# Kernel tuning notes

Measured on AMD Instinct MI355X. Metric: run time of the kernel, lower is better.

## Reference

```python
import jax, jax.numpy as jnp
import numpy as np


def setup_inputs() -> dict:
    key = jax.random.key(0)
    k1, k2, k3 = jax.random.split(key, 3)
    B, S, D, L = 8, 512, 512, 32
    head = jax.random.normal(k1, (B, S, D), dtype=jnp.float32)
    dep = jax.random.normal(k2, (B, S, D), dtype=jnp.float32)
    label_U_diag = jax.random.normal(k3, (L, D), dtype=jnp.float32)
    return {"head": head, "dep": dep, "label_U_diag": label_U_diag}


def reference(head, dep, label_U_diag):
    # head: [b, i, j], label_U_diag: [l, j], dep: [b, o, j] -> [b, l, i, o]
    return jnp.einsum('bij,lj,boj->blio', head, label_U_diag, dep)
```

## Files before the change

kernel.cpp:

```cpp
#include <hip/hip_runtime.h>
#include <hip/hip_bf16.h>

typedef float f32x4  __attribute__((ext_vector_type(4)));
typedef short bf16x8 __attribute__((ext_vector_type(8)));

__device__ __forceinline__ short bf16r(float x) {
    unsigned u = __builtin_bit_cast(unsigned, x);
    u += 0x7fffu + ((u >> 16) & 1u);
    return (short)(u >> 16);
}

__global__ void cvt_kernel(const float* __restrict__ head, const float* __restrict__ dep,
                           short* __restrict__ hb, short* __restrict__ db) {
    const int n8 = 8 * 512 * 512 / 8;
    int i = blockIdx.x * blockDim.x + threadIdx.x;
    const float* src = (i < n8) ? head : dep;
    short* dst = (i < n8) ? hb : db;
    int j = (i < n8) ? i : i - n8;
    f32x4 a = *(const f32x4*)(src + (size_t)j * 8);
    f32x4 c = *(const f32x4*)(src + (size_t)j * 8 + 4);
    bf16x8 v;
#pragma unroll
    for (int e = 0; e < 4; ++e) { v[e] = bf16r(a[e]); v[4 + e] = bf16r(c[e]); }
    *(bf16x8*)(dst + (size_t)j * 8) = v;
}

__global__ __launch_bounds__(512, 2)
void bla_gemm3(const short* __restrict__ headb,
               const short* __restrict__ depb,
               const float* __restrict__ U,
               float* __restrict__ out)
{
    constexpr int S = 512, D = 512, L = 32, BM = 256, BN = 256, BK = 64, NT = 8;

    __shared__ __align__(16) short Al[2][BM * BK];
    __shared__ __align__(16) short Bl[2][BN * BK];

    const int tid = threadIdx.x, lane = tid & 63, wid = tid >> 6;
    const int wm = wid >> 2, wn = wid & 3;

    const int swz = (blockIdx.x & 7) * ((int)gridDim.x >> 3) + (blockIdx.x >> 3);
    const int b = swz >> 7, rem = swz & 127;
    const int it = rem >> 6, l = (rem >> 1) & 31, ot = rem & 1;
    const int i0 = it * BM, o0 = ot * BN;

    const int ar = tid >> 3, ac = (tid & 7) * 8;
    const short* hbase = headb + (size_t)(b * S + i0 + ar) * D + ac;
    const float* ubase = U + (size_t)l * D + ac;
    const int awoff = ((((tid & 7) * 16) ^ ((ar & 7) << 4)) >> 1);

    const int bso = ((lane & 7) * 16) ^ ((lane >> 3) << 4);
    const short* dbase = depb + (size_t)(b * S + o0) * D;

    bf16x8 rA[4];
    float  ruf[8];

#define A_ISSUE(t_) do {                                                        \
        _Pragma("unroll")                                                       \
        for (int p = 0; p < 4; ++p)                                             \
            rA[p] = *(const bf16x8*)(hbase + (size_t)(p * 64) * D + (t_) * BK); \
        f32x4 u0 = *(const f32x4*)(ubase + (t_) * BK);                          \
        f32x4 u1 = *(const f32x4*)(ubase + (t_) * BK + 4);                      \
        _Pragma("unroll")                                                       \
        for (int e = 0; e < 4; ++e) { ruf[e] = u0[e]; ruf[4 + e] = u1[e]; }     \
    } while (0)

#define A_WRITE(buf_) do {                                                      \
        _Pragma("unroll")                                                       \
        for (int p = 0; p < 4; ++p) {                                           \
            bf16x8 av;                                                          \
            _Pragma("unroll")                                                   \
            for (int e = 0; e < 8; ++e) {                                       \
                float f = __builtin_bit_cast(float,                             \
                    (unsigned)((unsigned short)rA[p][e]) << 16) * ruf[e];       \
                av[e] = bf16r(f);                                               \
            }                                                                   \
            *(bf16x8*)&Al[buf_][(ar + p * 64) * BK + awoff] = av;               \
        }                                                                       \
    } while (0)

#define B_ISSUE(t_, buf_) do {                                                  \
        _Pragma("unroll")                                                       \
        for (int q = 0; q < 4; ++q) {                                           \
            const int rg = wid * 32 + q * 8 + (lane >> 3);                      \
            const char* s_ = (const char*)dbase +                               \
                ((size_t)rg * D + (size_t)(t_) * BK) * 2 + bso;                 \
            __builtin_amdgcn_global_load_lds(                                   \
                (const __attribute__((address_space(1))) void*)s_,              \
                (__attribute__((address_space(3))) void*)&Bl[buf_][(wid * 32 + q * 8) * BK], \
                16, 0, 0);                                                      \
        }                                                                       \
    } while (0)

    f32x4 acc[8][4] = {};
    bf16x8 bfr[4];

#define DSREAD_A(buf_, mh_, ks_, af_) do {                                      \
        const int cb = (ks_) * 64 + ((lane >> 4) << 4);                         \
        _Pragma("unroll")                                                       \
        for (int f = 0; f < 4; ++f) {                                           \
            const int row = wm * 128 + ((mh_) * 4 + f) * 16 + (lane & 15);      \
            af_[f] = *(const bf16x8*)&Al[buf_][row * BK + ((cb ^ ((row & 7) << 4)) >> 1)]; \
        }                                                                       \
    } while (0)

#define DSREAD_B(buf_, ks_) do {                                                \
        const int cb = (ks_) * 64 + ((lane >> 4) << 4);                         \
        _Pragma("unroll")                                                       \
        for (int f = 0; f < 4; ++f) {                                           \
            const int row = wn * 64 + f * 16 + (lane & 15);                     \
            bfr[f] = *(const bf16x8*)&Bl[buf_][row * BK + ((cb ^ ((row & 7) << 4)) >> 1)]; \
        }                                                                       \
    } while (0)

#define MFMA16(mh_, af_) do {                                                   \
        __builtin_amdgcn_s_setprio(1);                                          \
        _Pragma("unroll")                                                       \
        for (int m = 0; m < 4; ++m)                                             \
            _Pragma("unroll")                                                   \
            for (int n = 0; n < 4; ++n)                                         \
                acc[(mh_) * 4 + m][n] = __builtin_amdgcn_mfma_f32_16x16x32_bf16(\
                    af_[m], bfr[n], acc[(mh_) * 4 + m][n], 0, 0, 0);            \
        __builtin_amdgcn_s_setprio(0);                                          \
    } while (0)

#define SB()  __builtin_amdgcn_sched_barrier(0)
#define BAR() __builtin_amdgcn_s_barrier()

    A_ISSUE(0);
    B_ISSUE(0, 0);
    A_WRITE(0);
    asm volatile("s_waitcnt vmcnt(0) lgkmcnt(0)");
    BAR();

#pragma unroll
    for (int t = 0; t < NT; ++t) {
        const int c = t & 1;
        bf16x8 af[4];
        if (t < NT - 1) { A_ISSUE(t + 1); B_ISSUE(t + 1, c ^ 1); }
        DSREAD_A(c, 0, 0, af); DSREAD_B(c, 0);
        SB(); BAR();
        MFMA16(0, af);
        SB(); BAR();
        DSREAD_A(c, 1, 0, af);
        SB(); BAR();
        MFMA16(1, af);
        SB(); BAR();
        if (t < NT - 1) A_WRITE(c ^ 1);
        DSREAD_A(c, 0, 1, af); DSREAD_B(c, 1);
        SB(); BAR();
        MFMA16(0, af);
        SB(); BAR();
        DSREAD_A(c, 1, 1, af);
        SB(); BAR();
        MFMA16(1, af);
        SB();
        asm volatile("s_waitcnt vmcnt(0) lgkmcnt(0)");
        BAR();
    }

    float* op = out + (size_t)(b * L + l) * S * S;
#pragma unroll
    for (int m = 0; m < 8; ++m) {
        const int row0 = i0 + wm * 128 + m * 16 + ((lane >> 4) << 2);
#pragma unroll
        for (int n = 0; n < 4; ++n) {
            const int col = o0 + wn * 64 + n * 16 + (lane & 15);
#pragma unroll
            for (int r = 0; r < 4; ++r)
                op[(size_t)(row0 + r) * S + col] = acc[m][n][r];
        }
    }

#undef A_ISSUE
#undef A_WRITE
#undef B_ISSUE
#undef DSREAD_A
#undef DSREAD_B
#undef MFMA16
#undef SB
#undef BAR
}

__global__ __launch_bounds__(256, 2)
void bla_fb(const float* __restrict__ head, const float* __restrict__ dep,
            const float* __restrict__ U, float* __restrict__ out)
{
    constexpr int S = 512, D = 512, L = 32, BM = 128, BN = 128, BK = 64, NT = 8;
    __shared__ short Al[2][BM * BK];
    __shared__ short Bl[2][BN * BK];
    const int tid = threadIdx.x, lane = tid & 63, wid = tid >> 6;
    const int wm = wid >> 1, wn = wid & 1;
    const int swz = (blockIdx.x & 7) * ((int)gridDim.x >> 3) + (blockIdx.x >> 3);
    const int b = swz >> 9, rem = swz & 511;
    const int l = rem >> 4, it = (rem >> 2) & 3, ot = rem & 3;
    const int i0 = it * BM, o0 = ot * BN;
    const int srow = tid >> 3, scol = (tid & 7) * 8, swb = scol * 2;
    const float* hb = head + (size_t)(b * S + i0 + srow) * D + scol;
    const float* db = dep + (size_t)(b * S + o0 + srow) * D + scol;
    const float* ub = U + l * D + scol;
    f32x4 ra[4][2], rb[4][2], ru[2];
#define FSTAGE_LOAD(t) do { const int k0_ = (t) * BK;                              \
        ru[0] = *(const f32x4*)(ub + k0_); ru[1] = *(const f32x4*)(ub + k0_ + 4);  \
        _Pragma("unroll") for (int p_ = 0; p_ < 4; ++p_) {                         \
            ra[p_][0] = *(const f32x4*)(hb + k0_ + p_ * 32 * D);                   \
            ra[p_][1] = *(const f32x4*)(hb + k0_ + p_ * 32 * D + 4);               \
            rb[p_][0] = *(const f32x4*)(db + k0_ + p_ * 32 * D);                   \
            rb[p_][1] = *(const f32x4*)(db + k0_ + p_ * 32 * D + 4); } } while (0)
#define FSTAGE_WRITE(buf) do { _Pragma("unroll") for (int p_ = 0; p_ < 4; ++p_) {  \
            const int row_ = srow + p_ * 32; const int sb_ = swb ^ ((row_ & 7) << 4); \
            bf16x8 av_, bv_;                                                       \
            _Pragma("unroll") for (int q_ = 0; q_ < 2; ++q_)                       \
                _Pragma("unroll") for (int j_ = 0; j_ < 4; ++j_) {                 \
                    av_[q_ * 4 + j_] = bf16r(ra[p_][q_][j_] * ru[q_][j_]);         \
                    bv_[q_ * 4 + j_] = bf16r(rb[p_][q_][j_]); }                    \
            *(bf16x8*)&Al[buf][row_ * BK + (sb_ >> 1)] = av_;                      \
            *(bf16x8*)&Bl[buf][row_ * BK + (sb_ >> 1)] = bv_; } } while (0)
    f32x4 acc[4][4] = {};
    const int cbase = (lane >> 4) << 4, rsw = (lane & 7) << 4;
#define FCOMPUTE(buf) do { _Pragma("unroll") for (int ks_ = 0; ks_ < 2; ++ks_) {   \
            const int sb2_ = (ks_ * 64 + cbase) ^ rsw; bf16x8 af_[4], bfr_[4];     \
            _Pragma("unroll") for (int f_ = 0; f_ < 4; ++f_) {                     \
                af_[f_] = *(const bf16x8*)&Al[buf][(wm * 64 + f_ * 16 + (lane & 15)) * BK + (sb2_ >> 1)]; \
                bfr_[f_] = *(const bf16x8*)&Bl[buf][(wn * 64 + f_ * 16 + (lane & 15)) * BK + (sb2_ >> 1)]; } \
            _Pragma("unroll") for (int fm_ = 0; fm_ < 4; ++fm_)                    \
                _Pragma("unroll") for (int fn_ = 0; fn_ < 4; ++fn_)                \
                    acc[fm_][fn_] = __builtin_amdgcn_mfma_f32_16x16x32_bf16(       \
                        af_[fm_], bfr_[fn_], acc[fm_][fn_], 0, 0, 0); } } while (0)
    FSTAGE_LOAD(0); FSTAGE_WRITE(0); __syncthreads();
    int cur = 0;
#pragma unroll
    for (int t = 0; t < NT; ++t) {
        if (t + 1 < NT) FSTAGE_LOAD(t + 1);
        FCOMPUTE(cur);
        if (t + 1 < NT) FSTAGE_WRITE(cur ^ 1);
        __syncthreads();
        cur ^= 1;
    }
    float* op = out + (size_t)(b * L + l) * S * S;
#pragma unroll
    for (int fm = 0; fm < 4; ++fm) {
        const int row0 = i0 + wm * 64 + fm * 16 + ((lane >> 4) << 2);
#pragma unroll
        for (int fn = 0; fn < 4; ++fn) {
            const int col = o0 + wn * 64 + fn * 16 + (lane & 15);
#pragma unroll
            for (int r = 0; r < 4; ++r)
                op[(size_t)(row0 + r) * S + col] = acc[fm][fn][r];
        }
    }
#undef FSTAGE_LOAD
#undef FSTAGE_WRITE
#undef FCOMPUTE
}

extern "C" void kernel_launch(void* const* d_in, const int* in_sizes, int n_in,
                              void* d_out, int out_size, void* d_ws, size_t ws_size,
                              hipStream_t stream)
{
    const float* head = (const float*)d_in[0];
    const float* dep  = (const float*)d_in[1];
    const float* U    = (const float*)d_in[2];
    float* out        = (float*)d_out;

    const size_t nelem = (size_t)8 * 512 * 512;
    const size_t need  = nelem * 2 * 2;
    if (ws_size >= need) {
        short* headb = (short*)d_ws;
        short* depb  = headb + nelem;
        cvt_kernel<<<dim3(2048), dim3(256), 0, stream>>>(head, dep, headb, depb);
        bla_gemm3<<<dim3(1024), dim3(512), 0, stream>>>(headb, depb, U, out);
    } else {
        bla_fb<<<dim3(4096), dim3(256), 0, stream>>>(head, dep, U, out);
    }
}
```

Measured before the change: 127.3 us.

## Deepen A-operand register prefetch to two stages and interleave B loads with MFMA phases

The main GEMM now holds two register stages of head/U tiles, so global loads for tile t+2 are issued while tile t is computed. The B global-to-LDS loads and the A scale-and-write into LDS are split into halves and spread across the four MFMA phases of each iteration. The per-iteration wait becomes a partial vmcnt so the newest prefetch can stay in flight across the barrier. This aims to hide global-load latency behind the matrix cores, at the cost of higher register pressure and fragile hand-written wait counts. The bf16 rounding also switches to the __float2bfloat16 intrinsic.

```diff
diff --git a/kernel.cpp b/kernel.cpp
--- a/kernel.cpp
+++ b/kernel.cpp
@@ -26,7 +26,7 @@
 }
 
 __global__ __launch_bounds__(512, 2)
-void bla_gemm3(const short* __restrict__ headb,
+void bla_gemm4(const short* __restrict__ headb,
                const short* __restrict__ depb,
                const float* __restrict__ U,
                float* __restrict__ out)
@@ -52,42 +52,45 @@
     const int bso = ((lane & 7) * 16) ^ ((lane >> 3) << 4);
     const short* dbase = depb + (size_t)(b * S + o0) * D;
 
-    bf16x8 rA[4];
-    float  ruf[8];
-
-#define A_ISSUE(t_) do {                                                        \
+    bf16x8 rA[2][4];
+    f32x4  ru[2][2];
+
+#define SBAR() __builtin_amdgcn_sched_barrier(0)
+
+#define A_ISSUE(tt) do {                                                        \
+        const int s_ = (tt) & 1;                                                \
         _Pragma("unroll")                                                       \
         for (int p = 0; p < 4; ++p)                                             \
-            rA[p] = *(const bf16x8*)(hbase + (size_t)(p * 64) * D + (t_) * BK); \
-        f32x4 u0 = *(const f32x4*)(ubase + (t_) * BK);                          \
-        f32x4 u1 = *(const f32x4*)(ubase + (t_) * BK + 4);                      \
-        _Pragma("unroll")                                                       \
-        for (int e = 0; e < 4; ++e) { ruf[e] = u0[e]; ruf[4 + e] = u1[e]; }     \
-    } while (0)
-
-#define A_WRITE(buf_) do {                                                      \
-        _Pragma("unroll")                                                       \
-        for (int p = 0; p < 4; ++p) {                                           \
+            rA[s_][p] = *(const bf16x8*)(hbase + (size_t)(p * 64) * D + (tt) * BK); \
+        ru[s_][0] = *(const f32x4*)(ubase + (tt) * BK);                         \
+        ru[s_][1] = *(const f32x4*)(ubase + (tt) * BK + 4);                     \
+    } while (0)
+
+#define A_WRITE_H(tt, h) do {                                                   \
+        const int s_ = (tt) & 1;                                                \
+        _Pragma("unroll")                                                       \
+        for (int p = (h) * 2; p < (h) * 2 + 2; ++p) {                           \
             bf16x8 av;                                                          \
             _Pragma("unroll")                                                   \
             for (int e = 0; e < 8; ++e) {                                       \
                 float f = __builtin_bit_cast(float,                             \
-                    (unsigned)((unsigned short)rA[p][e]) << 16) * ruf[e];       \
-                av[e] = bf16r(f);                                               \
+                    (unsigned)((unsigned short)rA[s_][p][e]) << 16)             \
+                    * ru[s_][e >> 2][e & 3];                                    \
+                av[e] = __builtin_bit_cast(short, __float2bfloat16(f));         \
             }                                                                   \
-            *(bf16x8*)&Al[buf_][(ar + p * 64) * BK + awoff] = av;               \
-        }                                                                       \
-    } while (0)
-
-#define B_ISSUE(t_, buf_) do {                                                  \
-        _Pragma("unroll")                                                       \
-        for (int q = 0; q < 4; ++q) {                                           \
+            *(bf16x8*)&Al[s_][(ar + p * 64) * BK + awoff] = av;                 \
+        }                                                                       \
+    } while (0)
+
+#define B_ISSUE_H(tt, h) do {                                                   \
+        _Pragma("unroll")                                                       \
+        for (int q = (h) * 2; q < (h) * 2 + 2; ++q) {                           \
             const int rg = wid * 32 + q * 8 + (lane >> 3);                      \
             const char* s_ = (const char*)dbase +                               \
-                ((size_t)rg * D + (size_t)(t_) * BK) * 2 + bso;                 \
+                ((size_t)rg * D + (size_t)(tt) * BK) * 2 + bso;                 \
             __builtin_amdgcn_global_load_lds(                                   \
                 (const __attribute__((address_space(1))) void*)s_,              \
-                (__attribute__((address_space(3))) void*)&Bl[buf_][(wid * 32 + q * 8) * BK], \
+                (__attribute__((address_space(3))) void*)&Bl[(tt) & 1][(wid * 32 + q * 8) * BK], \
                 16, 0, 0);                                                      \
         }                                                                       \
     } while (0)
@@ -124,39 +127,54 @@
         __builtin_amdgcn_s_setprio(0);                                          \
     } while (0)
 
-#define SB()  __builtin_amdgcn_sched_barrier(0)
 #define BAR() __builtin_amdgcn_s_barrier()
 
     A_ISSUE(0);
-    B_ISSUE(0, 0);
-    A_WRITE(0);
-    asm volatile("s_waitcnt vmcnt(0) lgkmcnt(0)");
+    B_ISSUE_H(0, 0); B_ISSUE_H(0, 1);
+    SBAR();
+    A_WRITE_H(0, 0); A_WRITE_H(0, 1);
+    A_ISSUE(1);
+    SBAR();
+    asm volatile("s_waitcnt vmcnt(6) lgkmcnt(0)" ::: "memory");
+    SBAR();
     BAR();
+    SBAR();
 
 #pragma unroll
     for (int t = 0; t < NT; ++t) {
         const int c = t & 1;
         bf16x8 af[4];
-        if (t < NT - 1) { A_ISSUE(t + 1); B_ISSUE(t + 1, c ^ 1); }
+
         DSREAD_A(c, 0, 0, af); DSREAD_B(c, 0);
-        SB(); BAR();
+        if (t + 1 < NT) B_ISSUE_H(t + 1, 0);
+        SBAR(); BAR(); SBAR();
         MFMA16(0, af);
-        SB(); BAR();
+        SBAR(); BAR(); SBAR();
+
         DSREAD_A(c, 1, 0, af);
-        SB(); BAR();
+        if (t + 1 < NT) B_ISSUE_H(t + 1, 1);
+        SBAR(); BAR(); SBAR();
         MFMA16(1, af);
-        SB(); BAR();
-        if (t < NT - 1) A_WRITE(c ^ 1);
+        SBAR(); BAR(); SBAR();
+
         DSREAD_A(c, 0, 1, af); DSREAD_B(c, 1);
-        SB(); BAR();
+        if (t + 1 < NT) A_WRITE_H(t + 1, 0);
+        SBAR(); BAR(); SBAR();
         MFMA16(0, af);
-        SB(); BAR();
+        SBAR(); BAR(); SBAR();
+
         DSREAD_A(c, 1, 1, af);
-        SB(); BAR();
+        if (t + 1 < NT) A_WRITE_H(t + 1, 1);
+        if (t + 2 < NT) A_ISSUE(t + 2);
+        SBAR(); BAR(); SBAR();
         MFMA16(1, af);
-        SB();
-        asm volatile("s_waitcnt vmcnt(0) lgkmcnt(0)");
-        BAR();
+        SBAR();
+        if (t + 2 < NT) {
+            asm volatile("s_waitcnt vmcnt(6) lgkmcnt(0)" ::: "memory");
+        } else if (t + 1 < NT) {
+            asm volatile("s_waitcnt vmcnt(0) lgkmcnt(0)" ::: "memory");
+        }
+        SBAR(); BAR(); SBAR();
     }
 
     float* op = out + (size_t)(b * L + l) * S * S;
@@ -172,13 +190,13 @@
         }
     }
 
+#undef SBAR
 #undef A_ISSUE
-#undef A_WRITE
-#undef B_ISSUE
+#undef A_WRITE_H
+#undef B_ISSUE_H
 #undef DSREAD_A
 #undef DSREAD_B
 #undef MFMA16
-#undef SB
 #undef BAR
 }
 
@@ -269,7 +287,7 @@
         short* headb = (short*)d_ws;
         short* depb  = headb + nelem;
         cvt_kernel<<<dim3(2048), dim3(256), 0, stream>>>(head, dep, headb, depb);
-        bla_gemm3<<<dim3(1024), dim3(512), 0, stream>>>(headb, depb, U, out);
+        bla_gemm4<<<dim3(1024), dim3(512), 0, stream>>>(headb, depb, U, out);
     } else {
         bla_fb<<<dim3(4096), dim3(256), 0, stream>>>(head, dep, U, out);
     }
```

Measured after the change: 111.4 us. 12.5% less time.

## Load A fragments directly into registers, dropping A's LDS staging

Applied to the files above, without the earlier changes.

The A operand (head scaled by U[l]) is no longer written to shared memory. Each wave now loads its MFMA A fragments straight from global memory, scales them in registers and rounds to bf16. The wave layout changes to 4x2 with 64x128 per-wave tiles, so each wave reads more B fragments from LDS and reuses A across 8 columns. Most intra-iteration barriers are removed, leaving one per K-step. In exchange there are more scattered global loads for A, higher register pressure, and less latency hiding because every K-step waits on vmcnt(0).

```diff
diff --git a/kernel.cpp b/kernel.cpp
--- a/kernel.cpp
+++ b/kernel.cpp
@@ -26,160 +26,159 @@
 }
 
 __global__ __launch_bounds__(512, 2)
-void bla_gemm3(const short* __restrict__ headb,
+void bla_gemm6(const short* __restrict__ headb,
                const short* __restrict__ depb,
                const float* __restrict__ U,
                float* __restrict__ out)
 {
     constexpr int S = 512, D = 512, L = 32, BM = 256, BN = 256, BK = 64, NT = 8;
 
-    __shared__ __align__(16) short Al[2][BM * BK];
     __shared__ __align__(16) short Bl[2][BN * BK];
 
     const int tid = threadIdx.x, lane = tid & 63, wid = tid >> 6;
-    const int wm = wid >> 2, wn = wid & 3;
+    const int wm = wid >> 1, wn = wid & 1;
 
     const int swz = (blockIdx.x & 7) * ((int)gridDim.x >> 3) + (blockIdx.x >> 3);
     const int b = swz >> 7, rem = swz & 127;
     const int it = rem >> 6, l = (rem >> 1) & 31, ot = rem & 1;
     const int i0 = it * BM, o0 = ot * BN;
 
-    const int ar = tid >> 3, ac = (tid & 7) * 8;
-    const short* hbase = headb + (size_t)(b * S + i0 + ar) * D + ac;
-    const float* ubase = U + (size_t)l * D + ac;
-    const int awoff = ((((tid & 7) * 16) ^ ((ar & 7) << 4)) >> 1);
+    const short* hfrag = headb + (size_t)(b * S + i0 + wm * 64 + (lane & 15)) * D
+                         + ((lane >> 4) * 8);
+    const float* ubase = U + (size_t)l * D + ((lane >> 4) * 8);
 
     const int bso = ((lane & 7) * 16) ^ ((lane >> 3) << 4);
     const short* dbase = depb + (size_t)(b * S + o0) * D;
 
-    bf16x8 rA[4];
-    float  ruf[8];
-
-#define A_ISSUE(t_) do {                                                        \
-        _Pragma("unroll")                                                       \
-        for (int p = 0; p < 4; ++p)                                             \
-            rA[p] = *(const bf16x8*)(hbase + (size_t)(p * 64) * D + (t_) * BK); \
-        f32x4 u0 = *(const f32x4*)(ubase + (t_) * BK);                          \
-        f32x4 u1 = *(const f32x4*)(ubase + (t_) * BK + 4);                      \
-        _Pragma("unroll")                                                       \
-        for (int e = 0; e < 4; ++e) { ruf[e] = u0[e]; ruf[4 + e] = u1[e]; }     \
-    } while (0)
-
-#define A_WRITE(buf_) do {                                                      \
-        _Pragma("unroll")                                                       \
-        for (int p = 0; p < 4; ++p) {                                           \
-            bf16x8 av;                                                          \
-            _Pragma("unroll")                                                   \
-            for (int e = 0; e < 8; ++e) {                                       \
-                float f = __builtin_bit_cast(float,                             \
-                    (unsigned)((unsigned short)rA[p][e]) << 16) * ruf[e];       \
-                av[e] = bf16r(f);                                               \
-            }                                                                   \
-            *(bf16x8*)&Al[buf_][(ar + p * 64) * BK + awoff] = av;               \
-        }                                                                       \
-    } while (0)
-
-#define B_ISSUE(t_, buf_) do {                                                  \
+    bf16x8 rw[2][4];
+    bf16x8 sc[2][4];
+    f32x4  uf[2][2];
+    bf16x8 bfr[8];
+    f32x4  acc[4][8] = {};
+
+#define SB()  __builtin_amdgcn_sched_barrier(0)
+#define BAR() __builtin_amdgcn_s_barrier()
+
+#define B_ISSUE(tt) do {                                                        \
         _Pragma("unroll")                                                       \
         for (int q = 0; q < 4; ++q) {                                           \
             const int rg = wid * 32 + q * 8 + (lane >> 3);                      \
             const char* s_ = (const char*)dbase +                               \
-                ((size_t)rg * D + (size_t)(t_) * BK) * 2 + bso;                 \
+                ((size_t)rg * D + (size_t)(tt) * BK) * 2 + bso;                 \
             __builtin_amdgcn_global_load_lds(                                   \
                 (const __attribute__((address_space(1))) void*)s_,              \
-                (__attribute__((address_space(3))) void*)&Bl[buf_][(wid * 32 + q * 8) * BK], \
+                (__attribute__((address_space(3))) void*)&Bl[(tt) & 1][(wid * 32 + q * 8) * BK], \
                 16, 0, 0);                                                      \
         }                                                                       \
     } while (0)
 
-    f32x4 acc[8][4] = {};
-    bf16x8 bfr[4];
-
-#define DSREAD_A(buf_, mh_, ks_, af_) do {                                      \
-        const int cb = (ks_) * 64 + ((lane >> 4) << 4);                         \
-        _Pragma("unroll")                                                       \
-        for (int f = 0; f < 4; ++f) {                                           \
-            const int row = wm * 128 + ((mh_) * 4 + f) * 16 + (lane & 15);      \
-            af_[f] = *(const bf16x8*)&Al[buf_][row * BK + ((cb ^ ((row & 7) << 4)) >> 1)]; \
-        }                                                                       \
+#define AQ_ISSUE(tt, ks) do {                                                   \
+        _Pragma("unroll")                                                       \
+        for (int mf = 0; mf < 4; ++mf)                                          \
+            rw[ks][mf] = *(const bf16x8*)(hfrag + (size_t)(mf * 16) * D +       \
+                                          (tt) * BK + (ks) * 32);               \
+    } while (0)
+
+#define U_ISSUE(tt) do {                                                        \
+        _Pragma("unroll")                                                       \
+        for (int ks = 0; ks < 2; ++ks)                                          \
+            _Pragma("unroll")                                                   \
+            for (int h = 0; h < 2; ++h)                                         \
+                uf[ks][h] = *(const f32x4*)(ubase + (tt) * BK + ks * 32 + h * 4);\
+    } while (0)
+
+#define SCALE_ALL() do {                                                        \
+        _Pragma("unroll")                                                       \
+        for (int ks = 0; ks < 2; ++ks)                                          \
+            _Pragma("unroll")                                                   \
+            for (int mf = 0; mf < 4; ++mf) {                                    \
+                bf16x8 av;                                                      \
+                _Pragma("unroll")                                               \
+                for (int e = 0; e < 8; ++e) {                                   \
+                    float f = __builtin_bit_cast(float,                         \
+                        (unsigned)((unsigned short)rw[ks][mf][e]) << 16)        \
+                        * uf[ks][e >> 2][e & 3];                                \
+                    av[e] = __builtin_bit_cast(short, __float2bfloat16(f));     \
+                }                                                               \
+                sc[ks][mf] = av;                                                \
+            }                                                                   \
     } while (0)
 
 #define DSREAD_B(buf_, ks_) do {                                                \
         const int cb = (ks_) * 64 + ((lane >> 4) << 4);                         \
         _Pragma("unroll")                                                       \
-        for (int f = 0; f < 4; ++f) {                                           \
-            const int row = wn * 64 + f * 16 + (lane & 15);                     \
+        for (int f = 0; f < 8; ++f) {                                           \
+            const int row = wn * 128 + f * 16 + (lane & 15);                    \
             bfr[f] = *(const bf16x8*)&Bl[buf_][row * BK + ((cb ^ ((row & 7) << 4)) >> 1)]; \
         }                                                                       \
     } while (0)
 
-#define MFMA16(mh_, af_) do {                                                   \
+#define MFMA32(ks_) do {                                                        \
         __builtin_amdgcn_s_setprio(1);                                          \
         _Pragma("unroll")                                                       \
         for (int m = 0; m < 4; ++m)                                             \
             _Pragma("unroll")                                                   \
-            for (int n = 0; n < 4; ++n)                                         \
-                acc[(mh_) * 4 + m][n] = __builtin_amdgcn_mfma_f32_16x16x32_bf16(\
-                    af_[m], bfr[n], acc[(mh_) * 4 + m][n], 0, 0, 0);            \
+            for (int n = 0; n < 8; ++n)                                         \
+                acc[m][n] = __builtin_amdgcn_mfma_f32_16x16x32_bf16(            \
+                    sc[ks_][m], bfr[n], acc[m][n], 0, 0, 0);                    \
         __builtin_amdgcn_s_setprio(0);                                          \
     } while (0)
 
-#define SB()  __builtin_amdgcn_sched_barrier(0)
-#define BAR() __builtin_amdgcn_s_barrier()
-
-    A_ISSUE(0);
-    B_ISSUE(0, 0);
-    A_WRITE(0);
-    asm volatile("s_waitcnt vmcnt(0) lgkmcnt(0)");
+    B_ISSUE(0);
+    AQ_ISSUE(0, 0); AQ_ISSUE(0, 1); U_ISSUE(0);
+    SB();
+    SCALE_ALL();
+    SB();
+    asm volatile("s_waitcnt vmcnt(0)" ::: "memory");
+    SB();
     BAR();
 
 #pragma unroll
     for (int t = 0; t < NT; ++t) {
         const int c = t & 1;
-        bf16x8 af[4];
-        if (t < NT - 1) { A_ISSUE(t + 1); B_ISSUE(t + 1, c ^ 1); }
-        DSREAD_A(c, 0, 0, af); DSREAD_B(c, 0);
-        SB(); BAR();
-        MFMA16(0, af);
-        SB(); BAR();
-        DSREAD_A(c, 1, 0, af);
-        SB(); BAR();
-        MFMA16(1, af);
-        SB(); BAR();
-        if (t < NT - 1) A_WRITE(c ^ 1);
-        DSREAD_A(c, 0, 1, af); DSREAD_B(c, 1);
-        SB(); BAR();
-        MFMA16(0, af);
-        SB(); BAR();
-        DSREAD_A(c, 1, 1, af);
-        SB(); BAR();
-        MFMA16(1, af);
-        SB();
-        asm volatile("s_waitcnt vmcnt(0) lgkmcnt(0)");
-        BAR();
+
+        if (t + 1 < NT) { B_ISSUE(t + 1); AQ_ISSUE(t + 1, 0); }
+        SB();
+        DSREAD_B(c, 0);
+        SB();
+        MFMA32(0);
+        SB();
+        if (t + 1 < NT) { U_ISSUE(t + 1); AQ_ISSUE(t + 1, 1); }
+        SB();
+        DSREAD_B(c, 1);
+        SB();
+        MFMA32(1);
+        SB();
+        if (t + 1 < NT) {
+            SCALE_ALL();
+            SB();
+            asm volatile("s_waitcnt vmcnt(0)" ::: "memory");
+            SB();
+            BAR();
+        }
     }
 
     float* op = out + (size_t)(b * L + l) * S * S;
 #pragma unroll
-    for (int m = 0; m < 8; ++m) {
-        const int row0 = i0 + wm * 128 + m * 16 + ((lane >> 4) << 2);
-#pragma unroll
-        for (int n = 0; n < 4; ++n) {
-            const int col = o0 + wn * 64 + n * 16 + (lane & 15);
+    for (int m = 0; m < 4; ++m) {
+        const int row0 = i0 + wm * 64 + m * 16 + ((lane >> 4) << 2);
+#pragma unroll
+        for (int n = 0; n < 8; ++n) {
+            const int col = o0 + wn * 128 + n * 16 + (lane & 15);
 #pragma unroll
             for (int r = 0; r < 4; ++r)
                 op[(size_t)(row0 + r) * S + col] = acc[m][n][r];
         }
     }
 
-#undef A_ISSUE
-#undef A_WRITE
-#undef B_ISSUE
-#undef DSREAD_A
-#undef DSREAD_B
-#undef MFMA16
 #undef SB
 #undef BAR
+#undef B_ISSUE
+#undef AQ_ISSUE
+#undef U_ISSUE
+#undef SCALE_ALL
+#undef DSREAD_B
+#undef MFMA32
 }
 
 __global__ __launch_bounds__(256, 2)
@@ -269,7 +268,7 @@
         short* headb = (short*)d_ws;
         short* depb  = headb + nelem;
         cvt_kernel<<<dim3(2048), dim3(256), 0, stream>>>(head, dep, headb, depb);
-        bla_gemm3<<<dim3(1024), dim3(512), 0, stream>>>(headb, depb, U, out);
+        bla_gemm6<<<dim3(1024), dim3(512), 0, stream>>>(headb, depb, U, out);
     } else {
         bla_fb<<<dim3(4096), dim3(256), 0, stream>>>(head, dep, U, out);
     }
```

Measured after the change: 161.8 us. 27.0% more time.
